# Kernel optimization log

Hardware: AMD Instinct MI355X
Metric: run time of the kernel (lower is better)

## Reference

```python
import jax, jax.numpy as jnp
import numpy as np

N_NODES = 50000
N_EDGES = 800000
H, D_IN, D_OUT = 4, 256, 64


def setup_inputs() -> dict:
    key = jax.random.key(0)
    ks = jax.random.split(key, 7)
    x = jax.random.normal(ks[0], (N_NODES, D_IN), dtype=jnp.float32)
    idx = jax.random.randint(ks[1], (2, N_EDGES), 0, N_NODES, dtype=jnp.int32)
    elem = jax.random.uniform(ks[2], (N_EDGES,), dtype=jnp.float32)
    Ws = jax.random.normal(ks[3], (H, D_IN, D_OUT), dtype=jnp.float32) * 0.05
    bs = jax.random.normal(ks[4], (H, D_OUT), dtype=jnp.float32) * 0.05
    aw = jax.random.normal(ks[5], (H, 2 * D_OUT + 1), dtype=jnp.float32) * 0.05
    ab = jax.random.normal(ks[6], (H,), dtype=jnp.float32) * 0.05
    return {"x": x, "idx": idx, "elem": elem, "Ws": Ws, "bs": bs, "aw": aw, "ab": ab}


def reference(x, idx, elem, Ws, bs, aw, ab):
    N = x.shape[0]
    O = Ws.shape[-1]
    # per-head MLP (num_mlp_layers=1 -> single Linear): [H, N, O]
    feats = jnp.einsum('nd,hdo->hno', x, Ws) + bs[:, None, :]
    # attention linear on concat(src, dst, elem): split weights instead of
    # materializing the [E, 2O+1] concat; math is identical.
    aw_src, aw_dst, aw_e = aw[:, :O], aw[:, O:2 * O], aw[:, 2 * O]
    a_s = jnp.einsum('hno,ho->hn', feats, aw_src)   # [H, N]
    a_d = jnp.einsum('hno,ho->hn', feats, aw_dst)   # [H, N]
    src, dst = idx[0], idx[1]
    score = a_s[:, src] + a_d[:, dst] + aw_e[:, None] * elem[None, :] + ab[:, None]
    w = jnp.exp(-jax.nn.relu(score / 20.0))        # [H, E], in (0, 1]
    dst_f = feats[:, dst]                          # [H, E, O] gather
    seg = lambda vals: jax.ops.segment_sum(vals, src, num_segments=N)
    pooled = jax.vmap(lambda wi, fi: seg(wi[:, None] * fi))(w, dst_f)  # [H, N, O]
    row_sum = jax.vmap(lambda wi: seg(wi))(w)                          # [H, N]
    out = pooled / row_sum[:, :, None]
    # concat heads along feature dim: [N, H*O]
    return jnp.transpose(out, (1, 0, 2)).reshape(N, H * O)
```

## Files before the change

kernel.cpp:

```cpp
#include <hip/hip_runtime.h>
#include <math.h>

constexpr int DIN = 256;
constexpr int H   = 4;
constexpr int O   = 64;
constexpr int HO  = H * O;
constexpr int AWS = 2 * O + 1;
constexpr int BSH = 5;
constexpr int BINW = 1 << BSH;
constexpr int CAP = 768;
constexpr int HEB = 4096;

typedef __bf16 bf16x8 __attribute__((ext_vector_type(8)));
typedef __bf16 bf16x4 __attribute__((ext_vector_type(4)));
typedef float  f32x4  __attribute__((ext_vector_type(4)));

__device__ __forceinline__ float bf2f(unsigned short u) {
    union { unsigned int i; float f; } c;
    c.i = ((unsigned int)u) << 16;
    return c.f;
}

__global__ __launch_bounds__(256) void k_prep(const float* __restrict__ Ws,
    __bf16* __restrict__ Bt)
{
    const int i = blockIdx.x * 256 + threadIdx.x;
    const int k = i & 255;
    const int n = i >> 8;
    Bt[n * 256 + k] = (__bf16)Ws[(n >> 6) * (DIN * O) + k * O + (n & 63)];
}

__global__ __launch_bounds__(256) void k_gemm_hist(const float* __restrict__ x,
    const __bf16* __restrict__ Bt, const float* __restrict__ bs,
    const float* __restrict__ aw, int N, int GB,
    __bf16* __restrict__ F, float* __restrict__ a_sT, float* __restrict__ a_dT,
    const int* __restrict__ idx, int E, int* __restrict__ rank,
    int* __restrict__ hist, int NB, int NBIN)
{
    __shared__ union SM {
        __bf16 As[64][DIN + 8];
        int    lhist[64 * (DIN + 8) / 2];
    } sm;
    const int b = blockIdx.x;
    const int t = threadIdx.x;

    if (b >= GB) {
        for (int k = t; k < NBIN; k += 256) sm.lhist[k] = 0;
        __syncthreads();
        const int base_e = (b - GB) * HEB + t;
        #pragma unroll
        for (int i = 0; i < HEB / 256; ++i) {
            const int e = base_e + i * 256;
            if (e < E) {
                const int s = idx[e];
                rank[e] = atomicAdd(&sm.lhist[s >> BSH], 1);
            }
        }
        __syncthreads();
        const int bh = b - GB;
        for (int k = t; k < NBIN; k += 256)
            hist[(size_t)k * NB + bh] = sm.lhist[k];
        return;
    }

    const int w    = t >> 6;
    const int lane = t & 63;
    const int c15  = lane & 15;
    const int quad = lane >> 4;
    const int n0   = b * 64;

    #pragma unroll
    for (int i = 0; i < 16; ++i) {
        const int r   = i * 4 + w;
        const int row = n0 + r;
        float4 xv = make_float4(0.f, 0.f, 0.f, 0.f);
        if (row < N) xv = *(const float4*)&x[(size_t)row * DIN + lane * 4];
        bf16x4 pv = { (__bf16)xv.x, (__bf16)xv.y, (__bf16)xv.z, (__bf16)xv.w };
        *(bf16x4*)&sm.As[r][lane * 4] = pv;
    }
    __syncthreads();

    f32x4 acc[4][4] = {};
    const __bf16* BtW = Bt + (size_t)(w * 64) * 256;
    const int kq = quad * 8;

    #pragma unroll
    for (int k0 = 0; k0 < DIN; k0 += 32) {
        bf16x8 afr[4], bfr[4];
        #pragma unroll
        for (int rt = 0; rt < 4; ++rt)
            afr[rt] = *(const bf16x8*)&sm.As[rt * 16 + c15][k0 + kq];
        #pragma unroll
        for (int ct = 0; ct < 4; ++ct)
            bfr[ct] = *(const bf16x8*)&BtW[(size_t)(ct * 16 + c15) * 256 + k0 + kq];
        #pragma unroll
        for (int rt = 0; rt < 4; ++rt)
            #pragma unroll
            for (int ct = 0; ct < 4; ++ct)
                acc[rt][ct] = __builtin_amdgcn_mfma_f32_16x16x32_bf16(
                    afr[rt], bfr[ct], acc[rt][ct], 0, 0, 0);
    }

    const int h = w;
    float bsv[4], awsv[4], awdv[4];
    #pragma unroll
    for (int ct = 0; ct < 4; ++ct) {
        const int col = ct * 16 + c15;
        bsv[ct]  = bs[w * 64 + col];
        awsv[ct] = aw[h * AWS + col];
        awdv[ct] = aw[h * AWS + O + col];
    }

    #pragma unroll
    for (int rt = 0; rt < 4; ++rt) {
        float psum[4] = {0.f, 0.f, 0.f, 0.f};
        float pdum[4] = {0.f, 0.f, 0.f, 0.f};
        #pragma unroll
        for (int ct = 0; ct < 4; ++ct) {
            #pragma unroll
            for (int reg = 0; reg < 4; ++reg) {
                const float f = acc[rt][ct][reg] + bsv[ct];
                const int row = n0 + rt * 16 + quad * 4 + reg;
                if (row < N)
                    F[(size_t)row * HO + w * 64 + ct * 16 + c15] = (__bf16)f;
                psum[reg] = fmaf(f, awsv[ct], psum[reg]);
                pdum[reg] = fmaf(f, awdv[ct], pdum[reg]);
            }
        }
        #pragma unroll
        for (int reg = 0; reg < 4; ++reg) {
            float v = psum[reg], u = pdum[reg];
            #pragma unroll
            for (int off = 1; off < 16; off <<= 1) {
                v += __shfl_xor(v, off, 64);
                u += __shfl_xor(u, off, 64);
            }
            const int row = n0 + rt * 16 + quad * 4 + reg;
            if (c15 == 0 && row < N) {
                a_sT[row * H + h] = v;
                a_dT[row * H + h] = u;
            }
        }
    }
}

__global__ __launch_bounds__(256) void k_scan1(int* __restrict__ data,
    int* __restrict__ bsum, int T)
{
    __shared__ int wsum[4], woff[4];
    const int t = threadIdx.x, b = blockIdx.x;
    const int lane = t & 63, w = t >> 6;
    const int i0 = b * 1024 + t * 4;

    int4 v = make_int4(0, 0, 0, 0);
    if (i0 + 3 < T) v = *(const int4*)&data[i0];
    else {
        if (i0     < T) v.x = data[i0];
        if (i0 + 1 < T) v.y = data[i0 + 1];
        if (i0 + 2 < T) v.z = data[i0 + 2];
    }
    const int tot = v.x + v.y + v.z + v.w;
    int s = tot;
    #pragma unroll
    for (int off = 1; off < 64; off <<= 1) {
        const int u = __shfl_up(s, off, 64);
        if (lane >= off) s += u;
    }
    if (lane == 63) wsum[w] = s;
    __syncthreads();
    if (t == 0) {
        int run = 0;
        #pragma unroll
        for (int j = 0; j < 4; ++j) { woff[j] = run; run += wsum[j]; }
        bsum[b] = run;
    }
    __syncthreads();
    const int e0 = s - tot + woff[w];
    int4 o;
    o.x = e0; o.y = e0 + v.x; o.z = o.y + v.y; o.w = o.z + v.z;
    if (i0 + 3 < T) *(int4*)&data[i0] = o;
    else {
        if (i0     < T) data[i0]     = o.x;
        if (i0 + 1 < T) data[i0 + 1] = o.y;
        if (i0 + 2 < T) data[i0 + 2] = o.z;
    }
}

__global__ __launch_bounds__(256) void k_scan2(int* __restrict__ data, int n)
{
    __shared__ int wsum[4], woff[4];
    const int t = threadIdx.x;
    const int lane = t & 63, w = t >> 6;
    const int i0 = t * 4;

    int4 v = make_int4(0, 0, 0, 0);
    if (i0 + 3 < n) v = *(const int4*)&data[i0];
    else {
        if (i0     < n) v.x = data[i0];
        if (i0 + 1 < n) v.y = data[i0 + 1];
        if (i0 + 2 < n) v.z = data[i0 + 2];
    }
    const int tot = v.x + v.y + v.z + v.w;
    int s = tot;
    #pragma unroll
    for (int off = 1; off < 64; off <<= 1) {
        const int u = __shfl_up(s, off, 64);
        if (lane >= off) s += u;
    }
    if (lane == 63) wsum[w] = s;
    __syncthreads();
    if (t == 0) {
        int run = 0;
        #pragma unroll
        for (int j = 0; j < 4; ++j) { woff[j] = run; run += wsum[j]; }
    }
    __syncthreads();
    const int e0 = s - tot + woff[w];
    int4 o;
    o.x = e0; o.y = e0 + v.x; o.z = o.y + v.y; o.w = o.z + v.z;
    if (i0 + 3 < n) *(int4*)&data[i0] = o;
    else {
        if (i0     < n) data[i0]     = o.x;
        if (i0 + 1 < n) data[i0 + 1] = o.y;
        if (i0 + 2 < n) data[i0 + 2] = o.z;
    }
}

__global__ __launch_bounds__(256) void k_scatter(const int* __restrict__ idx,
    const float* __restrict__ elem, const int* __restrict__ rank,
    const int* __restrict__ hist, const int* __restrict__ hsum,
    int NB, int E, int2* __restrict__ csr)
{
    const int e = blockIdx.x * 256 + threadIdx.x;
    if (e >= E) return;
    const int s = idx[e];
    const int d = idx[E + e];
    const int i = (s >> BSH) * NB + (e / HEB);
    const int pos = hist[i] + hsum[i >> 10] + rank[e];
    csr[pos] = make_int2((int)(((unsigned)s << 16) | (unsigned)d),
                         __float_as_int(elem[e]));
}

__global__ __launch_bounds__(256) void k_bingather(const int* __restrict__ hist,
    const int* __restrict__ hsum, int NB, int NBIN, int N, int E,
    const float* __restrict__ a_sT, const float* __restrict__ a_dT,
    const float* __restrict__ aw, const float* __restrict__ ab,
    const int2* __restrict__ csr, const __bf16* __restrict__ F,
    float* __restrict__ out)
{
    __shared__ unsigned short ld[CAP];
    __shared__ float4 lw[CAP];
    __shared__ float4 s_as[BINW];
    __shared__ int h[BINW], cur[BINW], off_a[BINW + 1];

    const int k = blockIdx.x;
    const int t = threadIdx.x;
    const int wv = t >> 6, lane = t & 63;

    const int i0 = k * NB;
    const int S = hist[i0] + hsum[i0 >> 10];
    int Snext = E;
    if (k + 1 < NBIN) {
        const int i1 = (k + 1) * NB;
        Snext = hist[i1] + hsum[i1 >> 10];
    }
    int cnt = Snext - S;
    if (cnt > CAP) cnt = CAP;

    if (t < BINW) {
        h[t] = 0;
        const int node = k * BINW + t;
        s_as[t] = (node < N) ? *(const float4*)&a_sT[node * 4]
                             : make_float4(0.f, 0.f, 0.f, 0.f);
    }
    __syncthreads();

    for (int j = t; j < cnt; j += 256)
        atomicAdd(&h[((unsigned)csr[S + j].x >> 16) & (BINW - 1)], 1);
    __syncthreads();

    if (t < BINW) {
        const int v = h[t];
        int s = v;
        #pragma unroll
        for (int off = 1; off < BINW; off <<= 1) {
            const int u = __shfl_up(s, off, 64);
            if (t >= off) s += u;
        }
        const int excl = s - v;
        cur[t]   = excl;
        off_a[t] = excl;
        if (t == BINW - 1) off_a[BINW] = excl + v;
    }
    __syncthreads();

    const float4 ab4 = *(const float4*)&ab[0];
    const float4 awe4 = make_float4(aw[0 * AWS + 2 * O], aw[1 * AWS + 2 * O],
                                    aw[2 * AWS + 2 * O], aw[3 * AWS + 2 * O]);
    for (int j = t; j < cnt; j += 256) {
        const int2 r = csr[S + j];
        const unsigned sd = (unsigned)r.x;
        const int sl = (sd >> 16) & (BINW - 1);
        const int d  = (int)(sd & 0xFFFFu);
        const int pos = atomicAdd(&cur[sl], 1);
        const float el = __int_as_float(r.y);
        const float4 as = s_as[sl];
        const float4 ad = *(const float4*)&a_dT[d * 4];
        float4 w4;
        w4.x = __expf(-fmaxf((as.x + ad.x + awe4.x * el + ab4.x) * 0.05f, 0.f));
        w4.y = __expf(-fmaxf((as.y + ad.y + awe4.y * el + ab4.y) * 0.05f, 0.f));
        w4.z = __expf(-fmaxf((as.z + ad.z + awe4.z * el + ab4.z) * 0.05f, 0.f));
        w4.w = __expf(-fmaxf((as.w + ad.w + awe4.w * el + ab4.w) * 0.05f, 0.f));
        ld[pos] = (unsigned short)d;
        lw[pos] = w4;
    }
    __syncthreads();

    const int h16 = lane >> 4;
    const __bf16* __restrict__ Fl = F + lane * 4;
    const float* lwf = (const float*)&lw[0];

    for (int i = 0; i < BINW / 4; ++i) {
        const int nl = wv * (BINW / 4) + i;
        const int n  = k * BINW + nl;
        if (n >= N) continue;
        const int jb = off_a[nl];
        const int je = off_a[nl + 1];

        float4 acc = make_float4(0.f, 0.f, 0.f, 0.f);
        float  rs  = 0.f;
        int j = jb;
        for (; j + 8 <= je; j += 8) {
            int dd[8]; float ww[8]; ushort4 ff[8];
            #pragma unroll
            for (int q = 0; q < 8; ++q) {
                dd[q] = ld[j + q];
                ww[q] = lwf[(j + q) * 4 + h16];
            }
            #pragma unroll
            for (int q = 0; q < 8; ++q)
                ff[q] = *(const ushort4*)&Fl[(size_t)dd[q] * HO];
            #pragma unroll
            for (int q = 0; q < 8; ++q) {
                acc.x = fmaf(ww[q], bf2f(ff[q].x), acc.x);
                acc.y = fmaf(ww[q], bf2f(ff[q].y), acc.y);
                acc.z = fmaf(ww[q], bf2f(ff[q].z), acc.z);
                acc.w = fmaf(ww[q], bf2f(ff[q].w), acc.w);
                rs += ww[q];
            }
        }
        for (; j + 4 <= je; j += 4) {
            int dd[4]; float ww[4]; ushort4 ff[4];
            #pragma unroll
            for (int q = 0; q < 4; ++q) {
                dd[q] = ld[j + q];
                ww[q] = lwf[(j + q) * 4 + h16];
            }
            #pragma unroll
            for (int q = 0; q < 4; ++q)
                ff[q] = *(const ushort4*)&Fl[(size_t)dd[q] * HO];
            #pragma unroll
            for (int q = 0; q < 4; ++q) {
                acc.x = fmaf(ww[q], bf2f(ff[q].x), acc.x);
                acc.y = fmaf(ww[q], bf2f(ff[q].y), acc.y);
                acc.z = fmaf(ww[q], bf2f(ff[q].z), acc.z);
                acc.w = fmaf(ww[q], bf2f(ff[q].w), acc.w);
                rs += ww[q];
            }
        }
        for (; j < je; ++j) {
            const int d = ld[j];
            const float w = lwf[j * 4 + h16];
            const ushort4 fv = *(const ushort4*)&Fl[(size_t)d * HO];
            acc.x = fmaf(w, bf2f(fv.x), acc.x);
            acc.y = fmaf(w, bf2f(fv.y), acc.y);
            acc.z = fmaf(w, bf2f(fv.z), acc.z);
            acc.w = fmaf(w, bf2f(fv.w), acc.w);
            rs += w;
        }

        const float inv = 1.f / rs;
        float4 o = make_float4(acc.x * inv, acc.y * inv,
                               acc.z * inv, acc.w * inv);
        *(float4*)&out[(size_t)n * HO + lane * 4] = o;
    }
}

extern "C" void kernel_launch(void* const* d_in, const int* in_sizes, int n_in,
                              void* d_out, int out_size, void* d_ws, size_t ws_size,
                              hipStream_t stream)
{
    const float* x    = (const float*)d_in[0];
    const int*   idx  = (const int*)d_in[1];
    const float* elem = (const float*)d_in[2];
    const float* Ws   = (const float*)d_in[3];
    const float* bs   = (const float*)d_in[4];
    const float* aw   = (const float*)d_in[5];
    const float* ab   = (const float*)d_in[6];

    const int N    = in_sizes[0] / DIN;
    const int E    = in_sizes[1] / 2;
    const int GB   = (N + 63) / 64;
    const int NB   = (E + HEB - 1) / HEB;
    const int NBIN = (N + BINW - 1) / BINW;
    const int T    = NBIN * NB;
    const int nb1  = (T + 1023) / 1024;

    __bf16* F      = (__bf16*)d_ws;
    float* a_sT    = (float*)(F + (size_t)N * HO);
    float* a_dT    = a_sT + (size_t)N * H;
    int*   hist    = (int*)(a_dT + (size_t)N * H);
    int*   hsum    = hist + T;
    int*   rank    = hsum + (nb1 + 1);
    size_t off = (size_t)((char*)(rank + E) - (char*)d_ws);
    off = (off + 15) & ~(size_t)15;
    int2*  csr     = (int2*)((char*)d_ws + off);
    __bf16* Bt     = (__bf16*)(csr + E);
    float* out     = (float*)d_out;

    k_prep<<<256, 256, 0, stream>>>(Ws, Bt);
    k_gemm_hist<<<GB + NB, 256, 0, stream>>>(x, Bt, bs, aw, N, GB,
                                             F, a_sT, a_dT, idx, E,
                                             rank, hist, NB, NBIN);
    k_scan1<<<nb1, 256, 0, stream>>>(hist, hsum, T);
    k_scan2<<<1, 256, 0, stream>>>(hsum, nb1);
    k_scatter<<<(E + 255) / 256, 256, 0, stream>>>(idx, elem, rank, hist,
                                                   hsum, NB, E, csr);
    k_bingather<<<NBIN, 256, 0, stream>>>(hist, hsum, NB, NBIN, N, E,
                                          a_sT, a_dT, aw, ab, csr, F, out);
}
```

Baseline: 233.7 us.

## Fuse all stages into one persistent kernel with software grid barriers

Merges the prep, GEMM+histogram, scans, scatter and bin-gather kernels into a single persistent kernel with a fixed 768-block grid. Phases are separated by an atomic-counter grid barrier, the second-level scan is redone in each block's shared memory, and the barrier counter is cleared with a memset. This removes five kernel-launch boundaries and the gaps between them. In exchange it relies on all 768 blocks being co-resident, which risks deadlock if occupancy falls short, and the spin barriers and grid-stride loops can hurt load balance.

```diff
diff --git a/kernel.cpp b/kernel.cpp
--- a/kernel.cpp
+++ b/kernel.cpp
@@ -10,6 +10,17 @@
 constexpr int BINW = 1 << BSH;
 constexpr int CAP = 768;
 constexpr int HEB = 4096;
+constexpr int GRID = 768;
+
+constexpr int SMB    = 64 * (DIN + 8) * 2;
+constexpr int BG_LD  = 0;
+constexpr int BG_LW  = 1536;
+constexpr int BG_AS  = 13824;
+constexpr int BG_H   = 14336;
+constexpr int BG_CUR = 14464;
+constexpr int BG_OFF = 14592;
+constexpr int HS_OFF = 14736;
+constexpr int SC_OFF = 15952;
 
 typedef __bf16 bf16x8 __attribute__((ext_vector_type(8)));
 typedef __bf16 bf16x4 __attribute__((ext_vector_type(4)));
@@ -21,143 +32,42 @@
     return c.f;
 }
 
-__global__ __launch_bounds__(256) void k_prep(const float* __restrict__ Ws,
-    __bf16* __restrict__ Bt)
+__device__ __forceinline__ void gridbar(unsigned* cnt, unsigned* gen, unsigned G)
 {
-    const int i = blockIdx.x * 256 + threadIdx.x;
-    const int k = i & 255;
-    const int n = i >> 8;
-    Bt[n * 256 + k] = (__bf16)Ws[(n >> 6) * (DIN * O) + k * O + (n & 63)];
+    __syncthreads();
+    if (threadIdx.x == 0) {
+        const unsigned g = __hip_atomic_load(gen, __ATOMIC_RELAXED,
+                                             __HIP_MEMORY_SCOPE_AGENT);
+        __threadfence();
+        if (__hip_atomic_fetch_add(cnt, 1u, __ATOMIC_ACQ_REL,
+                                   __HIP_MEMORY_SCOPE_AGENT) == G - 1u) {
+            __hip_atomic_store(cnt, 0u, __ATOMIC_RELAXED,
+                               __HIP_MEMORY_SCOPE_AGENT);
+            __hip_atomic_fetch_add(gen, 1u, __ATOMIC_ACQ_REL,
+                                   __HIP_MEMORY_SCOPE_AGENT);
+        } else {
+            while (__hip_atomic_load(gen, __ATOMIC_ACQUIRE,
+                                     __HIP_MEMORY_SCOPE_AGENT) == g)
+                __builtin_amdgcn_s_sleep(2);
+        }
+        __threadfence();
+    }
+    __syncthreads();
 }
 
-__global__ __launch_bounds__(256) void k_gemm_hist(const float* __restrict__ x,
-    const __bf16* __restrict__ Bt, const float* __restrict__ bs,
-    const float* __restrict__ aw, int N, int GB,
-    __bf16* __restrict__ F, float* __restrict__ a_sT, float* __restrict__ a_dT,
-    const int* __restrict__ idx, int E, int* __restrict__ rank,
-    int* __restrict__ hist, int NB, int NBIN)
+__device__ __forceinline__ void local_scan(const int* __restrict__ bsum, int n,
+                                           int* hs, int* wsum)
 {
-    __shared__ union SM {
-        __bf16 As[64][DIN + 8];
-        int    lhist[64 * (DIN + 8) / 2];
-    } sm;
-    const int b = blockIdx.x;
+    int* woff = wsum + 4;
     const int t = threadIdx.x;
-
-    if (b >= GB) {
-        for (int k = t; k < NBIN; k += 256) sm.lhist[k] = 0;
-        __syncthreads();
-        const int base_e = (b - GB) * HEB + t;
-        #pragma unroll
-        for (int i = 0; i < HEB / 256; ++i) {
-            const int e = base_e + i * 256;
-            if (e < E) {
-                const int s = idx[e];
-                rank[e] = atomicAdd(&sm.lhist[s >> BSH], 1);
-            }
-        }
-        __syncthreads();
-        const int bh = b - GB;
-        for (int k = t; k < NBIN; k += 256)
-            hist[(size_t)k * NB + bh] = sm.lhist[k];
-        return;
-    }
-
-    const int w    = t >> 6;
-    const int lane = t & 63;
-    const int c15  = lane & 15;
-    const int quad = lane >> 4;
-    const int n0   = b * 64;
-
-    #pragma unroll
-    for (int i = 0; i < 16; ++i) {
-        const int r   = i * 4 + w;
-        const int row = n0 + r;
-        float4 xv = make_float4(0.f, 0.f, 0.f, 0.f);
-        if (row < N) xv = *(const float4*)&x[(size_t)row * DIN + lane * 4];
-        bf16x4 pv = { (__bf16)xv.x, (__bf16)xv.y, (__bf16)xv.z, (__bf16)xv.w };
-        *(bf16x4*)&sm.As[r][lane * 4] = pv;
-    }
-    __syncthreads();
-
-    f32x4 acc[4][4] = {};
-    const __bf16* BtW = Bt + (size_t)(w * 64) * 256;
-    const int kq = quad * 8;
-
-    #pragma unroll
-    for (int k0 = 0; k0 < DIN; k0 += 32) {
-        bf16x8 afr[4], bfr[4];
-        #pragma unroll
-        for (int rt = 0; rt < 4; ++rt)
-            afr[rt] = *(const bf16x8*)&sm.As[rt * 16 + c15][k0 + kq];
-        #pragma unroll
-        for (int ct = 0; ct < 4; ++ct)
-            bfr[ct] = *(const bf16x8*)&BtW[(size_t)(ct * 16 + c15) * 256 + k0 + kq];
-        #pragma unroll
-        for (int rt = 0; rt < 4; ++rt)
-            #pragma unroll
-            for (int ct = 0; ct < 4; ++ct)
-                acc[rt][ct] = __builtin_amdgcn_mfma_f32_16x16x32_bf16(
-                    afr[rt], bfr[ct], acc[rt][ct], 0, 0, 0);
-    }
-
-    const int h = w;
-    float bsv[4], awsv[4], awdv[4];
-    #pragma unroll
-    for (int ct = 0; ct < 4; ++ct) {
-        const int col = ct * 16 + c15;
-        bsv[ct]  = bs[w * 64 + col];
-        awsv[ct] = aw[h * AWS + col];
-        awdv[ct] = aw[h * AWS + O + col];
-    }
-
-    #pragma unroll
-    for (int rt = 0; rt < 4; ++rt) {
-        float psum[4] = {0.f, 0.f, 0.f, 0.f};
-        float pdum[4] = {0.f, 0.f, 0.f, 0.f};
-        #pragma unroll
-        for (int ct = 0; ct < 4; ++ct) {
-            #pragma unroll
-            for (int reg = 0; reg < 4; ++reg) {
-                const float f = acc[rt][ct][reg] + bsv[ct];
-                const int row = n0 + rt * 16 + quad * 4 + reg;
-                if (row < N)
-                    F[(size_t)row * HO + w * 64 + ct * 16 + c15] = (__bf16)f;
-                psum[reg] = fmaf(f, awsv[ct], psum[reg]);
-                pdum[reg] = fmaf(f, awdv[ct], pdum[reg]);
-            }
-        }
-        #pragma unroll
-        for (int reg = 0; reg < 4; ++reg) {
-            float v = psum[reg], u = pdum[reg];
-            #pragma unroll
-            for (int off = 1; off < 16; off <<= 1) {
-                v += __shfl_xor(v, off, 64);
-                u += __shfl_xor(u, off, 64);
-            }
-            const int row = n0 + rt * 16 + quad * 4 + reg;
-            if (c15 == 0 && row < N) {
-                a_sT[row * H + h] = v;
-                a_dT[row * H + h] = u;
-            }
-        }
-    }
-}
-
-__global__ __launch_bounds__(256) void k_scan1(int* __restrict__ data,
-    int* __restrict__ bsum, int T)
-{
-    __shared__ int wsum[4], woff[4];
-    const int t = threadIdx.x, b = blockIdx.x;
     const int lane = t & 63, w = t >> 6;
-    const int i0 = b * 1024 + t * 4;
-
+    const int i0 = t * 4;
     int4 v = make_int4(0, 0, 0, 0);
-    if (i0 + 3 < T) v = *(const int4*)&data[i0];
+    if (i0 + 3 < n) v = *(const int4*)&bsum[i0];
     else {
-        if (i0     < T) v.x = data[i0];
-        if (i0 + 1 < T) v.y = data[i0 + 1];
-        if (i0 + 2 < T) v.z = data[i0 + 2];
+        if (i0     < n) v.x = bsum[i0];
+        if (i0 + 1 < n) v.y = bsum[i0 + 1];
+        if (i0 + 2 < n) v.z = bsum[i0 + 2];
     }
     const int tot = v.x + v.y + v.z + v.w;
     int s = tot;
@@ -172,217 +82,346 @@
         int run = 0;
         #pragma unroll
         for (int j = 0; j < 4; ++j) { woff[j] = run; run += wsum[j]; }
-        bsum[b] = run;
     }
     __syncthreads();
     const int e0 = s - tot + woff[w];
-    int4 o;
-    o.x = e0; o.y = e0 + v.x; o.z = o.y + v.y; o.w = o.z + v.z;
-    if (i0 + 3 < T) *(int4*)&data[i0] = o;
-    else {
-        if (i0     < T) data[i0]     = o.x;
-        if (i0 + 1 < T) data[i0 + 1] = o.y;
-        if (i0 + 2 < T) data[i0 + 2] = o.z;
-    }
+    if (i0     < n) hs[i0]     = e0;
+    if (i0 + 1 < n) hs[i0 + 1] = e0 + v.x;
+    if (i0 + 2 < n) hs[i0 + 2] = e0 + v.x + v.y;
+    if (i0 + 3 < n) hs[i0 + 3] = e0 + v.x + v.y + v.z;
+    __syncthreads();
 }
 
-__global__ __launch_bounds__(256) void k_scan2(int* __restrict__ data, int n)
+__global__ __launch_bounds__(256, 4) void k_mega(
+    const float* __restrict__ x, const int* __restrict__ idx,
+    const float* __restrict__ elem, const float* __restrict__ Ws,
+    const float* __restrict__ bs, const float* __restrict__ aw,
+    const float* __restrict__ ab,
+    __bf16* __restrict__ F, float* __restrict__ a_sT, float* __restrict__ a_dT,
+    int* __restrict__ hist, int* __restrict__ bsum, int* __restrict__ rank,
+    int2* __restrict__ csr, __bf16* __restrict__ Bt, float* __restrict__ out,
+    unsigned* __restrict__ bar,
+    int N, int E, int GB, int NBh, int NBIN, int NB, int T, int nb1)
 {
-    __shared__ int wsum[4], woff[4];
+    __shared__ __align__(16) unsigned char smp[SMB];
     const int t = threadIdx.x;
-    const int lane = t & 63, w = t >> 6;
-    const int i0 = t * 4;
-
-    int4 v = make_int4(0, 0, 0, 0);
-    if (i0 + 3 < n) v = *(const int4*)&data[i0];
-    else {
-        if (i0     < n) v.x = data[i0];
-        if (i0 + 1 < n) v.y = data[i0 + 1];
-        if (i0 + 2 < n) v.z = data[i0 + 2];
-    }
-    const int tot = v.x + v.y + v.z + v.w;
-    int s = tot;
-    #pragma unroll
-    for (int off = 1; off < 64; off <<= 1) {
-        const int u = __shfl_up(s, off, 64);
-        if (lane >= off) s += u;
-    }
-    if (lane == 63) wsum[w] = s;
-    __syncthreads();
-    if (t == 0) {
-        int run = 0;
-        #pragma unroll
-        for (int j = 0; j < 4; ++j) { woff[j] = run; run += wsum[j]; }
-    }
-    __syncthreads();
-    const int e0 = s - tot + woff[w];
-    int4 o;
-    o.x = e0; o.y = e0 + v.x; o.z = o.y + v.y; o.w = o.z + v.z;
-    if (i0 + 3 < n) *(int4*)&data[i0] = o;
-    else {
-        if (i0     < n) data[i0]     = o.x;
-        if (i0 + 1 < n) data[i0 + 1] = o.y;
-        if (i0 + 2 < n) data[i0 + 2] = o.z;
-    }
-}
-
-__global__ __launch_bounds__(256) void k_scatter(const int* __restrict__ idx,
-    const float* __restrict__ elem, const int* __restrict__ rank,
-    const int* __restrict__ hist, const int* __restrict__ hsum,
-    int NB, int E, int2* __restrict__ csr)
-{
-    const int e = blockIdx.x * 256 + threadIdx.x;
-    if (e >= E) return;
-    const int s = idx[e];
-    const int d = idx[E + e];
-    const int i = (s >> BSH) * NB + (e / HEB);
-    const int pos = hist[i] + hsum[i >> 10] + rank[e];
-    csr[pos] = make_int2((int)(((unsigned)s << 16) | (unsigned)d),
-                         __float_as_int(elem[e]));
-}
-
-__global__ __launch_bounds__(256) void k_bingather(const int* __restrict__ hist,
-    const int* __restrict__ hsum, int NB, int NBIN, int N, int E,
-    const float* __restrict__ a_sT, const float* __restrict__ a_dT,
-    const float* __restrict__ aw, const float* __restrict__ ab,
-    const int2* __restrict__ csr, const __bf16* __restrict__ F,
-    float* __restrict__ out)
-{
-    __shared__ unsigned short ld[CAP];
-    __shared__ float4 lw[CAP];
-    __shared__ float4 s_as[BINW];
-    __shared__ int h[BINW], cur[BINW], off_a[BINW + 1];
-
-    const int k = blockIdx.x;
-    const int t = threadIdx.x;
-    const int wv = t >> 6, lane = t & 63;
-
-    const int i0 = k * NB;
-    const int S = hist[i0] + hsum[i0 >> 10];
-    int Snext = E;
-    if (k + 1 < NBIN) {
-        const int i1 = (k + 1) * NB;
-        Snext = hist[i1] + hsum[i1 >> 10];
-    }
-    int cnt = Snext - S;
-    if (cnt > CAP) cnt = CAP;
-
-    if (t < BINW) {
-        h[t] = 0;
-        const int node = k * BINW + t;
-        s_as[t] = (node < N) ? *(const float4*)&a_sT[node * 4]
-                             : make_float4(0.f, 0.f, 0.f, 0.f);
-    }
-    __syncthreads();
-
-    for (int j = t; j < cnt; j += 256)
-        atomicAdd(&h[((unsigned)csr[S + j].x >> 16) & (BINW - 1)], 1);
-    __syncthreads();
-
-    if (t < BINW) {
-        const int v = h[t];
-        int s = v;
-        #pragma unroll
-        for (int off = 1; off < BINW; off <<= 1) {
-            const int u = __shfl_up(s, off, 64);
-            if (t >= off) s += u;
+    const unsigned G = (unsigned)gridDim.x;
+
+    for (int task = blockIdx.x; task < 256 + NBh; task += gridDim.x) {
+        __syncthreads();
+        if (task < 256) {
+            const int i = task * 256 + t;
+            const int k = i & 255;
+            const int n = i >> 8;
+            Bt[n * 256 + k] = (__bf16)Ws[(n >> 6) * (DIN * O) + k * O + (n & 63)];
+        } else {
+            int* lhist = (int*)smp;
+            for (int k2 = t; k2 < NBIN; k2 += 256) lhist[k2] = 0;
+            __syncthreads();
+            const int bh = task - 256;
+            const int base_e = bh * HEB + t;
+            #pragma unroll
+            for (int i = 0; i < HEB / 256; ++i) {
+                const int e = base_e + i * 256;
+                if (e < E) rank[e] = atomicAdd(&lhist[idx[e] >> BSH], 1);
+            }
+            __syncthreads();
+            for (int k2 = t; k2 < NBIN; k2 += 256)
+                hist[(size_t)k2 * NB + bh] = lhist[k2];
         }
-        const int excl = s - v;
-        cur[t]   = excl;
-        off_a[t] = excl;
-        if (t == BINW - 1) off_a[BINW] = excl + v;
-    }
-    __syncthreads();
-
-    const float4 ab4 = *(const float4*)&ab[0];
-    const float4 awe4 = make_float4(aw[0 * AWS + 2 * O], aw[1 * AWS + 2 * O],
-                                    aw[2 * AWS + 2 * O], aw[3 * AWS + 2 * O]);
-    for (int j = t; j < cnt; j += 256) {
-        const int2 r = csr[S + j];
-        const unsigned sd = (unsigned)r.x;
-        const int sl = (sd >> 16) & (BINW - 1);
-        const int d  = (int)(sd & 0xFFFFu);
-        const int pos = atomicAdd(&cur[sl], 1);
-        const float el = __int_as_float(r.y);
-        const float4 as = s_as[sl];
-        const float4 ad = *(const float4*)&a_dT[d * 4];
-        float4 w4;
-        w4.x = __expf(-fmaxf((as.x + ad.x + awe4.x * el + ab4.x) * 0.05f, 0.f));
-        w4.y = __expf(-fmaxf((as.y + ad.y + awe4.y * el + ab4.y) * 0.05f, 0.f));
-        w4.z = __expf(-fmaxf((as.z + ad.z + awe4.z * el + ab4.z) * 0.05f, 0.f));
-        w4.w = __expf(-fmaxf((as.w + ad.w + awe4.w * el + ab4.w) * 0.05f, 0.f));
-        ld[pos] = (unsigned short)d;
-        lw[pos] = w4;
-    }
-    __syncthreads();
-
-    const int h16 = lane >> 4;
-    const __bf16* __restrict__ Fl = F + lane * 4;
-    const float* lwf = (const float*)&lw[0];
-
-    for (int i = 0; i < BINW / 4; ++i) {
-        const int nl = wv * (BINW / 4) + i;
-        const int n  = k * BINW + nl;
-        if (n >= N) continue;
-        const int jb = off_a[nl];
-        const int je = off_a[nl + 1];
-
-        float4 acc = make_float4(0.f, 0.f, 0.f, 0.f);
-        float  rs  = 0.f;
-        int j = jb;
-        for (; j + 8 <= je; j += 8) {
-            int dd[8]; float ww[8]; ushort4 ff[8];
-            #pragma unroll
-            for (int q = 0; q < 8; ++q) {
-                dd[q] = ld[j + q];
-                ww[q] = lwf[(j + q) * 4 + h16];
-            }
-            #pragma unroll
-            for (int q = 0; q < 8; ++q)
-                ff[q] = *(const ushort4*)&Fl[(size_t)dd[q] * HO];
-            #pragma unroll
-            for (int q = 0; q < 8; ++q) {
-                acc.x = fmaf(ww[q], bf2f(ff[q].x), acc.x);
-                acc.y = fmaf(ww[q], bf2f(ff[q].y), acc.y);
-                acc.z = fmaf(ww[q], bf2f(ff[q].z), acc.z);
-                acc.w = fmaf(ww[q], bf2f(ff[q].w), acc.w);
-                rs += ww[q];
+        __syncthreads();
+    }
+    gridbar(&bar[0], &bar[1], G);
+
+    for (int task = blockIdx.x; task < GB + nb1; task += gridDim.x) {
+        __syncthreads();
+        if (task < GB) {
+            auto As = reinterpret_cast<__bf16 (*)[DIN + 8]>(smp);
+            const int b    = task;
+            const int w    = t >> 6;
+            const int lane = t & 63;
+            const int c15  = lane & 15;
+            const int quad = lane >> 4;
+            const int n0   = b * 64;
+
+            #pragma unroll
+            for (int i = 0; i < 16; ++i) {
+                const int r   = i * 4 + w;
+                const int row = n0 + r;
+                float4 xv = make_float4(0.f, 0.f, 0.f, 0.f);
+                if (row < N) xv = *(const float4*)&x[(size_t)row * DIN + lane * 4];
+                bf16x4 pv = { (__bf16)xv.x, (__bf16)xv.y, (__bf16)xv.z, (__bf16)xv.w };
+                *(bf16x4*)&As[r][lane * 4] = pv;
+            }
+            __syncthreads();
+
+            f32x4 acc[4][4] = {};
+            const __bf16* BtW = Bt + (size_t)(w * 64) * 256;
+            const int kq = quad * 8;
+
+            #pragma unroll
+            for (int k0 = 0; k0 < DIN; k0 += 32) {
+                bf16x8 afr[4], bfr[4];
+                #pragma unroll
+                for (int rt = 0; rt < 4; ++rt)
+                    afr[rt] = *(const bf16x8*)&As[rt * 16 + c15][k0 + kq];
+                #pragma unroll
+                for (int ct = 0; ct < 4; ++ct)
+                    bfr[ct] = *(const bf16x8*)&BtW[(size_t)(ct * 16 + c15) * 256 + k0 + kq];
+                #pragma unroll
+                for (int rt = 0; rt < 4; ++rt)
+                    #pragma unroll
+                    for (int ct = 0; ct < 4; ++ct)
+                        acc[rt][ct] = __builtin_amdgcn_mfma_f32_16x16x32_bf16(
+                            afr[rt], bfr[ct], acc[rt][ct], 0, 0, 0);
+            }
+
+            float bsv[4], awsv[4], awdv[4];
+            #pragma unroll
+            for (int ct = 0; ct < 4; ++ct) {
+                const int col = ct * 16 + c15;
+                bsv[ct]  = bs[w * 64 + col];
+                awsv[ct] = aw[w * AWS + col];
+                awdv[ct] = aw[w * AWS + O + col];
+            }
+
+            #pragma unroll
+            for (int rt = 0; rt < 4; ++rt) {
+                float psum[4] = {0.f, 0.f, 0.f, 0.f};
+                float pdum[4] = {0.f, 0.f, 0.f, 0.f};
+                #pragma unroll
+                for (int ct = 0; ct < 4; ++ct) {
+                    #pragma unroll
+                    for (int reg = 0; reg < 4; ++reg) {
+                        const float f = acc[rt][ct][reg] + bsv[ct];
+                        const int row = n0 + rt * 16 + quad * 4 + reg;
+                        if (row < N)
+                            F[(size_t)row * HO + w * 64 + ct * 16 + c15] = (__bf16)f;
+                        psum[reg] = fmaf(f, awsv[ct], psum[reg]);
+                        pdum[reg] = fmaf(f, awdv[ct], pdum[reg]);
+                    }
+                }
+                #pragma unroll
+                for (int reg = 0; reg < 4; ++reg) {
+                    float v = psum[reg], u = pdum[reg];
+                    #pragma unroll
+                    for (int off = 1; off < 16; off <<= 1) {
+                        v += __shfl_xor(v, off, 64);
+                        u += __shfl_xor(u, off, 64);
+                    }
+                    const int row = n0 + rt * 16 + quad * 4 + reg;
+                    if (c15 == 0 && row < N) {
+                        a_sT[row * H + w] = v;
+                        a_dT[row * H + w] = u;
+                    }
+                }
+            }
+        } else {
+            const int bsc = task - GB;
+            int* wsum = (int*)(smp + SC_OFF);
+            int* woff = wsum + 4;
+            const int lane = t & 63, w = t >> 6;
+            const int i0 = bsc * 1024 + t * 4;
+            int4 v = make_int4(0, 0, 0, 0);
+            if (i0 + 3 < T) v = *(const int4*)&hist[i0];
+            else {
+                if (i0     < T) v.x = hist[i0];
+                if (i0 + 1 < T) v.y = hist[i0 + 1];
+                if (i0 + 2 < T) v.z = hist[i0 + 2];
+            }
+            const int tot = v.x + v.y + v.z + v.w;
+            int s = tot;
+            #pragma unroll
+            for (int off = 1; off < 64; off <<= 1) {
+                const int u = __shfl_up(s, off, 64);
+                if (lane >= off) s += u;
+            }
+            if (lane == 63) wsum[w] = s;
+            __syncthreads();
+            if (t == 0) {
+                int run = 0;
+                #pragma unroll
+                for (int j = 0; j < 4; ++j) { woff[j] = run; run += wsum[j]; }
+                bsum[bsc] = run;
+            }
+            __syncthreads();
+            const int e0 = s - tot + woff[w];
+            int4 o;
+            o.x = e0; o.y = e0 + v.x; o.z = o.y + v.y; o.w = o.z + v.z;
+            if (i0 + 3 < T) *(int4*)&hist[i0] = o;
+            else {
+                if (i0     < T) hist[i0]     = o.x;
+                if (i0 + 1 < T) hist[i0 + 1] = o.y;
+                if (i0 + 2 < T) hist[i0 + 2] = o.z;
             }
         }
-        for (; j + 4 <= je; j += 4) {
-            int dd[4]; float ww[4]; ushort4 ff[4];
-            #pragma unroll
-            for (int q = 0; q < 4; ++q) {
-                dd[q] = ld[j + q];
-                ww[q] = lwf[(j + q) * 4 + h16];
-            }
-            #pragma unroll
-            for (int q = 0; q < 4; ++q)
-                ff[q] = *(const ushort4*)&Fl[(size_t)dd[q] * HO];
-            #pragma unroll
-            for (int q = 0; q < 4; ++q) {
-                acc.x = fmaf(ww[q], bf2f(ff[q].x), acc.x);
-                acc.y = fmaf(ww[q], bf2f(ff[q].y), acc.y);
-                acc.z = fmaf(ww[q], bf2f(ff[q].z), acc.z);
-                acc.w = fmaf(ww[q], bf2f(ff[q].w), acc.w);
-                rs += ww[q];
+        __syncthreads();
+    }
+    gridbar(&bar[0], &bar[1], G);
+
+    {
+        int* hs  = (int*)(smp + HS_OFF);
+        int* wsc = (int*)(smp + SC_OFF);
+        local_scan(bsum, nb1, hs, wsc);
+        const int TOTC = (E + 255) >> 8;
+        for (int task = blockIdx.x; task < TOTC; task += gridDim.x) {
+            const int e = task * 256 + t;
+            if (e < E) {
+                const int s = idx[e];
+                const int d = idx[E + e];
+                const int i = (s >> BSH) * NB + (e / HEB);
+                const int pos = hist[i] + hs[i >> 10] + rank[e];
+                csr[pos] = make_int2((int)(((unsigned)s << 16) | (unsigned)d),
+                                     __float_as_int(elem[e]));
             }
         }
-        for (; j < je; ++j) {
-            const int d = ld[j];
-            const float w = lwf[j * 4 + h16];
-            const ushort4 fv = *(const ushort4*)&Fl[(size_t)d * HO];
-            acc.x = fmaf(w, bf2f(fv.x), acc.x);
-            acc.y = fmaf(w, bf2f(fv.y), acc.y);
-            acc.z = fmaf(w, bf2f(fv.z), acc.z);
-            acc.w = fmaf(w, bf2f(fv.w), acc.w);
-            rs += w;
+    }
+    gridbar(&bar[0], &bar[1], G);
+
+    {
+        int* hs  = (int*)(smp + HS_OFF);
+        int* wsc = (int*)(smp + SC_OFF);
+        local_scan(bsum, nb1, hs, wsc);
+
+        unsigned short* ld_ = (unsigned short*)(smp + BG_LD);
+        float4* lw    = (float4*)(smp + BG_LW);
+        float4* s_as  = (float4*)(smp + BG_AS);
+        int*    h     = (int*)(smp + BG_H);
+        int*    cur   = (int*)(smp + BG_CUR);
+        int*    off_a = (int*)(smp + BG_OFF);
+
+        const int wv = t >> 6, lane = t & 63;
+        const int h16 = lane >> 4;
+        const float4 ab4 = *(const float4*)&ab[0];
+        const float4 awe4 = make_float4(aw[0 * AWS + 2 * O], aw[1 * AWS + 2 * O],
+                                        aw[2 * AWS + 2 * O], aw[3 * AWS + 2 * O]);
+        const __bf16* __restrict__ Fl = F + lane * 4;
+        const float* lwf = (const float*)lw;
+
+        for (int k = blockIdx.x; k < NBIN; k += gridDim.x) {
+            __syncthreads();
+            const int i0 = k * NB;
+            const int S = hist[i0] + hs[i0 >> 10];
+            int Snext = E;
+            if (k + 1 < NBIN) {
+                const int i1 = (k + 1) * NB;
+                Snext = hist[i1] + hs[i1 >> 10];
+            }
+            int bcnt = Snext - S;
+            if (bcnt > CAP) bcnt = CAP;
+
+            if (t < BINW) {
+                h[t] = 0;
+                const int node = k * BINW + t;
+                s_as[t] = (node < N) ? *(const float4*)&a_sT[node * 4]
+                                     : make_float4(0.f, 0.f, 0.f, 0.f);
+            }
+            __syncthreads();
+
+            for (int j = t; j < bcnt; j += 256)
+                atomicAdd(&h[((unsigned)csr[S + j].x >> 16) & (BINW - 1)], 1);
+            __syncthreads();
+
+            if (t < BINW) {
+                const int v = h[t];
+                int s = v;
+                #pragma unroll
+                for (int off = 1; off < BINW; off <<= 1) {
+                    const int u = __shfl_up(s, off, 64);
+                    if (t >= off) s += u;
+                }
+                const int excl = s - v;
+                cur[t]   = excl;
+                off_a[t] = excl;
+                if (t == BINW - 1) off_a[BINW] = excl + v;
+            }
+            __syncthreads();
+
+            for (int j = t; j < bcnt; j += 256) {
+                const int2 r = csr[S + j];
+                const unsigned sd = (unsigned)r.x;
+                const int sl = (sd >> 16) & (BINW - 1);
+                const int d  = (int)(sd & 0xFFFFu);
+                const int pos = atomicAdd(&cur[sl], 1);
+                const float el = __int_as_float(r.y);
+                const float4 as = s_as[sl];
+                const float4 ad = *(const float4*)&a_dT[d * 4];
+                float4 w4;
+                w4.x = __expf(-fmaxf((as.x + ad.x + awe4.x * el + ab4.x) * 0.05f, 0.f));
+                w4.y = __expf(-fmaxf((as.y + ad.y + awe4.y * el + ab4.y) * 0.05f, 0.f));
+                w4.z = __expf(-fmaxf((as.z + ad.z + awe4.z * el + ab4.z) * 0.05f, 0.f));
+                w4.w = __expf(-fmaxf((as.w + ad.w + awe4.w * el + ab4.w) * 0.05f, 0.f));
+                ld_[pos] = (unsigned short)d;
+                lw[pos]  = w4;
+            }
+            __syncthreads();
+
+            for (int i = 0; i < BINW / 4; ++i) {
+                const int nl = wv * (BINW / 4) + i;
+                const int n  = k * BINW + nl;
+                if (n >= N) continue;
+                const int jb = off_a[nl];
+                const int je = off_a[nl + 1];
+
+                float4 acc = make_float4(0.f, 0.f, 0.f, 0.f);
+                float  rs  = 0.f;
+                int j = jb;
+                for (; j + 8 <= je; j += 8) {
+                    int dd[8]; float ww[8]; ushort4 ff[8];
+                    #pragma unroll
+                    for (int q = 0; q < 8; ++q) {
+                        dd[q] = ld_[j + q];
+                        ww[q] = lwf[(j + q) * 4 + h16];
+                    }
+                    #pragma unroll
+                    for (int q = 0; q < 8; ++q)
+                        ff[q] = *(const ushort4*)&Fl[(size_t)dd[q] * HO];
+                    #pragma unroll
+                    for (int q = 0; q < 8; ++q) {
+                        acc.x = fmaf(ww[q], bf2f(ff[q].x), acc.x);
+                        acc.y = fmaf(ww[q], bf2f(ff[q].y), acc.y);
+                        acc.z = fmaf(ww[q], bf2f(ff[q].z), acc.z);
+                        acc.w = fmaf(ww[q], bf2f(ff[q].w), acc.w);
+                        rs += ww[q];
+                    }
+                }
+                for (; j + 4 <= je; j += 4) {
+                    int dd[4]; float ww[4]; ushort4 ff[4];
+                    #pragma unroll
+                    for (int q = 0; q < 4; ++q) {
+                        dd[q] = ld_[j + q];
+                        ww[q] = lwf[(j + q) * 4 + h16];
+                    }
+                    #pragma unroll
+                    for (int q = 0; q < 4; ++q)
+                        ff[q] = *(const ushort4*)&Fl[(size_t)dd[q] * HO];
+                    #pragma unroll
+                    for (int q = 0; q < 4; ++q) {
+                        acc.x = fmaf(ww[q], bf2f(ff[q].x), acc.x);
+                        acc.y = fmaf(ww[q], bf2f(ff[q].y), acc.y);
+                        acc.z = fmaf(ww[q], bf2f(ff[q].z), acc.z);
+                        acc.w = fmaf(ww[q], bf2f(ff[q].w), acc.w);
+                        rs += ww[q];
+                    }
+                }
+                for (; j < je; ++j) {
+                    const int d = ld_[j];
+                    const float w = lwf[j * 4 + h16];
+                    const ushort4 fv = *(const ushort4*)&Fl[(size_t)d * HO];
+                    acc.x = fmaf(w, bf2f(fv.x), acc.x);
+                    acc.y = fmaf(w, bf2f(fv.y), acc.y);
+                    acc.z = fmaf(w, bf2f(fv.z), acc.z);
+                    acc.w = fmaf(w, bf2f(fv.w), acc.w);
+                    rs += w;
+                }
+
+                const float inv = 1.f / rs;
+                float4 o = make_float4(acc.x * inv, acc.y * inv,
+                                       acc.z * inv, acc.w * inv);
+                *(float4*)&out[(size_t)n * HO + lane * 4] = o;
+            }
+            __syncthreads();
         }
-
-        const float inv = 1.f / rs;
-        float4 o = make_float4(acc.x * inv, acc.y * inv,
-                               acc.z * inv, acc.w * inv);
-        *(float4*)&out[(size_t)n * HO + lane * 4] = o;
     }
 }
 
@@ -401,31 +440,27 @@
     const int N    = in_sizes[0] / DIN;
     const int E    = in_sizes[1] / 2;
     const int GB   = (N + 63) / 64;
-    const int NB   = (E + HEB - 1) / HEB;
+    const int NBh  = (E + HEB - 1) / HEB;
     const int NBIN = (N + BINW - 1) / BINW;
-    const int T    = NBIN * NB;
+    const int T    = NBIN * NBh;
     const int nb1  = (T + 1023) / 1024;
 
-    __bf16* F      = (__bf16*)d_ws;
+    unsigned* bar  = (unsigned*)d_ws;
+    __bf16* F      = (__bf16*)((char*)d_ws + 16);
     float* a_sT    = (float*)(F + (size_t)N * HO);
     float* a_dT    = a_sT + (size_t)N * H;
     int*   hist    = (int*)(a_dT + (size_t)N * H);
-    int*   hsum    = hist + T;
-    int*   rank    = hsum + (nb1 + 1);
+    int*   bsum    = hist + ((T + 3) & ~3);
+    int*   rank    = bsum + ((nb1 + 4) & ~3);
     size_t off = (size_t)((char*)(rank + E) - (char*)d_ws);
     off = (off + 15) & ~(size_t)15;
     int2*  csr     = (int2*)((char*)d_ws + off);
     __bf16* Bt     = (__bf16*)(csr + E);
     float* out     = (float*)d_out;
 
-    k_prep<<<256, 256, 0, stream>>>(Ws, Bt);
-    k_gemm_hist<<<GB + NB, 256, 0, stream>>>(x, Bt, bs, aw, N, GB,
-                                             F, a_sT, a_dT, idx, E,
-                                             rank, hist, NB, NBIN);
-    k_scan1<<<nb1, 256, 0, stream>>>(hist, hsum, T);
-    k_scan2<<<1, 256, 0, stream>>>(hsum, nb1);
-    k_scatter<<<(E + 255) / 256, 256, 0, stream>>>(idx, elem, rank, hist,
-                                                   hsum, NB, E, csr);
-    k_bingather<<<NBIN, 256, 0, stream>>>(hist, hsum, NB, NBIN, N, E,
-                                          a_sT, a_dT, aw, ab, csr, F, out);
+    hipMemsetAsync(d_ws, 0, 16, stream);
+    k_mega<<<GRID, 256, 0, stream>>>(x, idx, elem, Ws, bs, aw, ab,
+                                     F, a_sT, a_dT, hist, bsum, rank,
+                                     csr, Bt, out, bar,
+                                     N, E, GB, NBh, NBIN, NBh, T, nb1);
 }
```

Result: slower. 874.6 us (+274.2%).

## Restructure pipeline to merge prep with histogram and gemm with scan, drop scan2

Applied to the files above, without the earlier changes.

The weight-transpose prep now shares a launch with the edge histogram, and the first-level scan of histogram counts runs as extra blocks of the GEMM kernel. The separate second-level scan kernel is removed. Instead, each scatter and bingather block redoes the small scan of block sums in shared memory. This cuts two kernel launches and their serialization gaps. In exchange, every block in the scatter and bingather kernels does redundant scan work and adds a few block-wide barriers.

```diff
diff --git a/kernel.cpp b/kernel.cpp
--- a/kernel.cpp
+++ b/kernel.cpp
@@ -21,45 +21,123 @@
     return c.f;
 }
 
-__global__ __launch_bounds__(256) void k_prep(const float* __restrict__ Ws,
-    __bf16* __restrict__ Bt)
-{
-    const int i = blockIdx.x * 256 + threadIdx.x;
-    const int k = i & 255;
-    const int n = i >> 8;
-    Bt[n * 256 + k] = (__bf16)Ws[(n >> 6) * (DIN * O) + k * O + (n & 63)];
-}
-
-__global__ __launch_bounds__(256) void k_gemm_hist(const float* __restrict__ x,
+__device__ __forceinline__ void local_scan(const int* __restrict__ bsum, int n,
+                                           int* hs, int* wsum)
+{
+    int* woff = wsum + 4;
+    const int t = threadIdx.x;
+    const int lane = t & 63, w = t >> 6;
+    const int i0 = t * 4;
+    int4 v = make_int4(0, 0, 0, 0);
+    if (i0 + 3 < n) v = *(const int4*)&bsum[i0];
+    else {
+        if (i0     < n) v.x = bsum[i0];
+        if (i0 + 1 < n) v.y = bsum[i0 + 1];
+        if (i0 + 2 < n) v.z = bsum[i0 + 2];
+    }
+    const int tot = v.x + v.y + v.z + v.w;
+    int s = tot;
+    #pragma unroll
+    for (int off = 1; off < 64; off <<= 1) {
+        const int u = __shfl_up(s, off, 64);
+        if (lane >= off) s += u;
+    }
+    if (lane == 63) wsum[w] = s;
+    __syncthreads();
+    if (t == 0) {
+        int run = 0;
+        #pragma unroll
+        for (int j = 0; j < 4; ++j) { woff[j] = run; run += wsum[j]; }
+    }
+    __syncthreads();
+    const int e0 = s - tot + woff[w];
+    if (i0     < n) hs[i0]     = e0;
+    if (i0 + 1 < n) hs[i0 + 1] = e0 + v.x;
+    if (i0 + 2 < n) hs[i0 + 2] = e0 + v.x + v.y;
+    if (i0 + 3 < n) hs[i0 + 3] = e0 + v.x + v.y + v.z;
+    __syncthreads();
+}
+
+__global__ __launch_bounds__(256) void k_prep_hist(const float* __restrict__ Ws,
+    __bf16* __restrict__ Bt, const int* __restrict__ idx, int E,
+    int* __restrict__ rank, int* __restrict__ hist, int NB, int NBIN)
+{
+    __shared__ int lhist[2048];
+    const int b = blockIdx.x, t = threadIdx.x;
+
+    if (b < 256) {
+        const int i = b * 256 + t;
+        const int k = i & 255;
+        const int n = i >> 8;
+        Bt[n * 256 + k] = (__bf16)Ws[(n >> 6) * (DIN * O) + k * O + (n & 63)];
+        return;
+    }
+
+    const int bh = b - 256;
+    for (int k = t; k < NBIN; k += 256) lhist[k] = 0;
+    __syncthreads();
+    const int base_e = bh * HEB + t;
+    #pragma unroll
+    for (int i = 0; i < HEB / 256; ++i) {
+        const int e = base_e + i * 256;
+        if (e < E) rank[e] = atomicAdd(&lhist[idx[e] >> BSH], 1);
+    }
+    __syncthreads();
+    for (int k = t; k < NBIN; k += 256)
+        hist[(size_t)k * NB + bh] = lhist[k];
+}
+
+__global__ __launch_bounds__(256) void k_gemm_scan(const float* __restrict__ x,
     const __bf16* __restrict__ Bt, const float* __restrict__ bs,
     const float* __restrict__ aw, int N, int GB,
     __bf16* __restrict__ F, float* __restrict__ a_sT, float* __restrict__ a_dT,
-    const int* __restrict__ idx, int E, int* __restrict__ rank,
-    int* __restrict__ hist, int NB, int NBIN)
+    int* __restrict__ hist, int* __restrict__ bsum, int T)
 {
     __shared__ union SM {
         __bf16 As[64][DIN + 8];
-        int    lhist[64 * (DIN + 8) / 2];
+        int    scr[8];
     } sm;
     const int b = blockIdx.x;
     const int t = threadIdx.x;
 
     if (b >= GB) {
-        for (int k = t; k < NBIN; k += 256) sm.lhist[k] = 0;
+        const int bsc = b - GB;
+        int* wsum = sm.scr;
+        int* woff = wsum + 4;
+        const int lane = t & 63, w = t >> 6;
+        const int i0 = bsc * 1024 + t * 4;
+        int4 v = make_int4(0, 0, 0, 0);
+        if (i0 + 3 < T) v = *(const int4*)&hist[i0];
+        else {
+            if (i0     < T) v.x = hist[i0];
+            if (i0 + 1 < T) v.y = hist[i0 + 1];
+            if (i0 + 2 < T) v.z = hist[i0 + 2];
+        }
+        const int tot = v.x + v.y + v.z + v.w;
+        int s = tot;
+        #pragma unroll
+        for (int off = 1; off < 64; off <<= 1) {
+            const int u = __shfl_up(s, off, 64);
+            if (lane >= off) s += u;
+        }
+        if (lane == 63) wsum[w] = s;
         __syncthreads();
-        const int base_e = (b - GB) * HEB + t;
-        #pragma unroll
-        for (int i = 0; i < HEB / 256; ++i) {
-            const int e = base_e + i * 256;
-            if (e < E) {
-                const int s = idx[e];
-                rank[e] = atomicAdd(&sm.lhist[s >> BSH], 1);
-            }
+        if (t == 0) {
+            int run = 0;
+            #pragma unroll
+            for (int j = 0; j < 4; ++j) { woff[j] = run; run += wsum[j]; }
+            bsum[bsc] = run;
         }
         __syncthreads();
-        const int bh = b - GB;
-        for (int k = t; k < NBIN; k += 256)
-            hist[(size_t)k * NB + bh] = sm.lhist[k];
+        const int e0 = s - tot + woff[w];
+        int4 o;
+        o.x = e0; o.y = e0 + v.x; o.z = o.y + v.y; o.w = o.z + v.z;
+        if (i0 + 3 < T) *(int4*)&hist[i0] = o;
+        else {
+            if (i0     < T) hist[i0]     = o.x;
+            if (i0 + 1 < T) hist[i0 + 1] = o.y;
+            if (i0 + 2 < T) hist[i0 + 2] = o.z;
+        }
         return;
     }
 
@@ -101,14 +179,13 @@
                     afr[rt], bfr[ct], acc[rt][ct], 0, 0, 0);
     }
 
-    const int h = w;
     float bsv[4], awsv[4], awdv[4];
     #pragma unroll
     for (int ct = 0; ct < 4; ++ct) {
         const int col = ct * 16 + c15;
         bsv[ct]  = bs[w * 64 + col];
-        awsv[ct] = aw[h * AWS + col];
-        awdv[ct] = aw[h * AWS + O + col];
+        awsv[ct] = aw[w * AWS + col];
+        awdv[ct] = aw[w * AWS + O + col];
     }
 
     #pragma unroll
@@ -137,132 +214,58 @@
             }
             const int row = n0 + rt * 16 + quad * 4 + reg;
             if (c15 == 0 && row < N) {
-                a_sT[row * H + h] = v;
-                a_dT[row * H + h] = u;
-            }
-        }
-    }
-}
-
-__global__ __launch_bounds__(256) void k_scan1(int* __restrict__ data,
-    int* __restrict__ bsum, int T)
-{
-    __shared__ int wsum[4], woff[4];
-    const int t = threadIdx.x, b = blockIdx.x;
-    const int lane = t & 63, w = t >> 6;
-    const int i0 = b * 1024 + t * 4;
-
-    int4 v = make_int4(0, 0, 0, 0);
-    if (i0 + 3 < T) v = *(const int4*)&data[i0];
-    else {
-        if (i0     < T) v.x = data[i0];
-        if (i0 + 1 < T) v.y = data[i0 + 1];
-        if (i0 + 2 < T) v.z = data[i0 + 2];
-    }
-    const int tot = v.x + v.y + v.z + v.w;
-    int s = tot;
-    #pragma unroll
-    for (int off = 1; off < 64; off <<= 1) {
-        const int u = __shfl_up(s, off, 64);
-        if (lane >= off) s += u;
-    }
-    if (lane == 63) wsum[w] = s;
-    __syncthreads();
-    if (t == 0) {
-        int run = 0;
-        #pragma unroll
-        for (int j = 0; j < 4; ++j) { woff[j] = run; run += wsum[j]; }
-        bsum[b] = run;
-    }
-    __syncthreads();
-    const int e0 = s - tot + woff[w];
-    int4 o;
-    o.x = e0; o.y = e0 + v.x; o.z = o.y + v.y; o.w = o.z + v.z;
-    if (i0 + 3 < T) *(int4*)&data[i0] = o;
-    else {
-        if (i0     < T) data[i0]     = o.x;
-        if (i0 + 1 < T) data[i0 + 1] = o.y;
-        if (i0 + 2 < T) data[i0 + 2] = o.z;
-    }
-}
-
-__global__ __launch_bounds__(256) void k_scan2(int* __restrict__ data, int n)
-{
-    __shared__ int wsum[4], woff[4];
-    const int t = threadIdx.x;
-    const int lane = t & 63, w = t >> 6;
-    const int i0 = t * 4;
-
-    int4 v = make_int4(0, 0, 0, 0);
-    if (i0 + 3 < n) v = *(const int4*)&data[i0];
-    else {
-        if (i0     < n) v.x = data[i0];
-        if (i0 + 1 < n) v.y = data[i0 + 1];
-        if (i0 + 2 < n) v.z = data[i0 + 2];
-    }
-    const int tot = v.x + v.y + v.z + v.w;
-    int s = tot;
-    #pragma unroll
-    for (int off = 1; off < 64; off <<= 1) {
-        const int u = __shfl_up(s, off, 64);
-        if (lane >= off) s += u;
-    }
-    if (lane == 63) wsum[w] = s;
-    __syncthreads();
-    if (t == 0) {
-        int run = 0;
-        #pragma unroll
-        for (int j = 0; j < 4; ++j) { woff[j] = run; run += wsum[j]; }
-    }
-    __syncthreads();
-    const int e0 = s - tot + woff[w];
-    int4 o;
-    o.x = e0; o.y = e0 + v.x; o.z = o.y + v.y; o.w = o.z + v.z;
-    if (i0 + 3 < n) *(int4*)&data[i0] = o;
-    else {
-        if (i0     < n) data[i0]     = o.x;
-        if (i0 + 1 < n) data[i0 + 1] = o.y;
-        if (i0 + 2 < n) data[i0 + 2] = o.z;
+                a_sT[row * H + w] = v;
+                a_dT[row * H + w] = u;
+            }
+        }
     }
 }
 
 __global__ __launch_bounds__(256) void k_scatter(const int* __restrict__ idx,
     const float* __restrict__ elem, const int* __restrict__ rank,
-    const int* __restrict__ hist, const int* __restrict__ hsum,
+    const int* __restrict__ hist, const int* __restrict__ bsum, int nb1,
     int NB, int E, int2* __restrict__ csr)
 {
+    __shared__ int hs[1024];
+    __shared__ int wsc[8];
+    local_scan(bsum, nb1, hs, wsc);
+
     const int e = blockIdx.x * 256 + threadIdx.x;
     if (e >= E) return;
     const int s = idx[e];
     const int d = idx[E + e];
     const int i = (s >> BSH) * NB + (e / HEB);
-    const int pos = hist[i] + hsum[i >> 10] + rank[e];
+    const int pos = hist[i] + hs[i >> 10] + rank[e];
     csr[pos] = make_int2((int)(((unsigned)s << 16) | (unsigned)d),
                          __float_as_int(elem[e]));
 }
 
 __global__ __launch_bounds__(256) void k_bingather(const int* __restrict__ hist,
-    const int* __restrict__ hsum, int NB, int NBIN, int N, int E,
+    const int* __restrict__ bsum, int nb1, int NB, int NBIN, int N, int E,
     const float* __restrict__ a_sT, const float* __restrict__ a_dT,
     const float* __restrict__ aw, const float* __restrict__ ab,
     const int2* __restrict__ csr, const __bf16* __restrict__ F,
     float* __restrict__ out)
 {
+    __shared__ int hs[1024];
+    __shared__ int wsc[8];
     __shared__ unsigned short ld[CAP];
     __shared__ float4 lw[CAP];
     __shared__ float4 s_as[BINW];
     __shared__ int h[BINW], cur[BINW], off_a[BINW + 1];
 
+    local_scan(bsum, nb1, hs, wsc);
+
     const int k = blockIdx.x;
     const int t = threadIdx.x;
     const int wv = t >> 6, lane = t & 63;
 
     const int i0 = k * NB;
-    const int S = hist[i0] + hsum[i0 >> 10];
+    const int S = hist[i0] + hs[i0 >> 10];
     int Snext = E;
     if (k + 1 < NBIN) {
         const int i1 = (k + 1) * NB;
-        Snext = hist[i1] + hsum[i1 >> 10];
+        Snext = hist[i1] + hs[i1 >> 10];
     }
     int cnt = Snext - S;
     if (cnt > CAP) cnt = CAP;
@@ -410,22 +413,20 @@
     float* a_sT    = (float*)(F + (size_t)N * HO);
     float* a_dT    = a_sT + (size_t)N * H;
     int*   hist    = (int*)(a_dT + (size_t)N * H);
-    int*   hsum    = hist + T;
-    int*   rank    = hsum + (nb1 + 1);
+    int*   bsum    = hist + ((T + 3) & ~3);
+    int*   rank    = bsum + ((nb1 + 4) & ~3);
     size_t off = (size_t)((char*)(rank + E) - (char*)d_ws);
     off = (off + 15) & ~(size_t)15;
     int2*  csr     = (int2*)((char*)d_ws + off);
     __bf16* Bt     = (__bf16*)(csr + E);
     float* out     = (float*)d_out;
 
-    k_prep<<<256, 256, 0, stream>>>(Ws, Bt);
-    k_gemm_hist<<<GB + NB, 256, 0, stream>>>(x, Bt, bs, aw, N, GB,
-                                             F, a_sT, a_dT, idx, E,
-                                             rank, hist, NB, NBIN);
-    k_scan1<<<nb1, 256, 0, stream>>>(hist, hsum, T);
-    k_scan2<<<1, 256, 0, stream>>>(hsum, nb1);
+    k_prep_hist<<<256 + NB, 256, 0, stream>>>(Ws, Bt, idx, E, rank,
+                                              hist, NB, NBIN);
+    k_gemm_scan<<<GB + nb1, 256, 0, stream>>>(x, Bt, bs, aw, N, GB,
+                                              F, a_sT, a_dT, hist, bsum, T);
     k_scatter<<<(E + 255) / 256, 256, 0, stream>>>(idx, elem, rank, hist,
-                                                   hsum, NB, E, csr);
-    k_bingather<<<NBIN, 256, 0, stream>>>(hist, hsum, NB, NBIN, N, E,
+                                                   bsum, nb1, NB, E, csr);
+    k_bingather<<<NBIN, 256, 0, stream>>>(hist, bsum, nb1, NB, NBIN, N, E,
                                           a_sT, a_dT, aw, ab, csr, F, out);
 }
```

New measurement: 236.5 us. No clear change (+1.2%).
